# Kernel optimization log

Hardware: AMD Instinct MI355X
Metric: run time of the kernel (lower is better)

Reference implementation:

```python
import jax, jax.numpy as jnp
import numpy as np

B, T, C = 2, 2048, 1024
H = 16
HD = C // H  # head_size = 64


def setup_inputs() -> dict:
    key = jax.random.key(0)
    k1, k2, k3 = jax.random.split(key, 3)
    x = jax.random.normal(k1, (B, T, C), dtype=jnp.float32)
    W_qkv = jax.random.normal(k2, (C, 3 * C), dtype=jnp.float32) * (1.0 / np.sqrt(C))
    b_qkv = jnp.zeros((3 * C,), dtype=jnp.float32)
    W_proj = jax.random.normal(k3, (C, C), dtype=jnp.float32) * (1.0 / np.sqrt(C))
    b_proj = jnp.zeros((C,), dtype=jnp.float32)
    return {"x": x, "W_qkv": W_qkv, "b_qkv": b_qkv, "W_proj": W_proj, "b_proj": b_proj}


def reference(x, W_qkv, b_qkv, W_proj, b_proj):
    Bc, Tc, Cc = x.shape
    qkv = x @ W_qkv + b_qkv                      # [B,T,3C]
    # Faithful to torch: view(B,T,H,3*HD) then chunk(3,-1) -> per-head interleaved split
    qkv = qkv.reshape(Bc, Tc, H, 3 * HD)
    q = qkv[..., 0 * HD:1 * HD]                  # [B,T,H,HD]
    k = qkv[..., 1 * HD:2 * HD]
    v = qkv[..., 2 * HD:3 * HD]
    # scores: [B,H,T,T]
    att = jnp.einsum('bqhd,bkhd->bhqk', q, k) / np.sqrt(HD)
    causal = jnp.tril(jnp.ones((Tc, Tc), dtype=bool))
    att = jnp.where(causal[None, None, :, :], att, -jnp.inf)
    att = jax.nn.softmax(att, axis=-1)
    out = jnp.einsum('bhqk,bkhd->bqhd', att, v).reshape(Bc, Tc, Cc)
    return out @ W_proj + b_proj
```

## Files before the change

### kernel.cpp

```cpp
#include <hip/hip_runtime.h>
#include <hip/hip_bf16.h>
#include <stdint.h>
#include <math.h>

#define T_SEQ 2048
#define NHEAD 16
#define CDIM 1024
#define QKV2_LD 2048

typedef __attribute__((ext_vector_type(8))) short short8;
typedef __attribute__((ext_vector_type(4))) short short4v;
typedef __attribute__((ext_vector_type(4))) float floatx4;

static __device__ __forceinline__ short bf16b(float f) {
    __hip_bfloat16 h = __float2bfloat16(f);
    return __builtin_bit_cast(short, h);
}

__device__ __forceinline__ void transpose_body(
    const float* __restrict__ in, __hip_bfloat16* __restrict__ out,
    int R, int C, int bx, int by, int tid)
{
    __shared__ short tile[64][65];
    const int r0 = by << 6;
    const int c0 = bx << 6;
    #pragma unroll
    for (int t = 0; t < 4; ++t) {
        int ch = t * 256 + tid;
        int rr = ch >> 4, cc = (ch & 15) << 2;
        float4 v = *(const float4*)(in + (size_t)(r0 + rr) * C + c0 + cc);
        tile[rr][cc + 0] = bf16b(v.x);
        tile[rr][cc + 1] = bf16b(v.y);
        tile[rr][cc + 2] = bf16b(v.z);
        tile[rr][cc + 3] = bf16b(v.w);
    }
    __syncthreads();
    #pragma unroll
    for (int t = 0; t < 2; ++t) {
        int ch = t * 256 + tid;
        int cc = ch >> 3, rr8 = (ch & 7) << 3;
        short8 v;
        #pragma unroll
        for (int j = 0; j < 8; ++j) v[j] = tile[rr8 + j][cc];
        *(short8*)(out + (size_t)(c0 + cc) * R + r0 + rr8) = v;
    }
}

__global__ __launch_bounds__(256) void prep_kernel(
    const float* __restrict__ x,     __hip_bfloat16* __restrict__ xb,
    const float* __restrict__ Wqkv,  __hip_bfloat16* __restrict__ WqkvT,
    const float* __restrict__ Wproj, __hip_bfloat16* __restrict__ WprojT)
{
    const int bid = blockIdx.x;
    const int tid = threadIdx.x;
    if (bid < 2048) {
        int i = (bid * 256 + tid) * 8;
        float4 a = *(const float4*)(x + i);
        float4 b = *(const float4*)(x + i + 4);
        short8 o;
        o[0] = bf16b(a.x); o[1] = bf16b(a.y); o[2] = bf16b(a.z); o[3] = bf16b(a.w);
        o[4] = bf16b(b.x); o[5] = bf16b(b.y); o[6] = bf16b(b.z); o[7] = bf16b(b.w);
        *(short8*)(xb + i) = o;
    } else if (bid < 2816) {
        int r = bid - 2048;
        transpose_body(Wqkv, WqkvT, 1024, 3072, r % 48, r / 48, tid);
    } else {
        int r = bid - 2816;
        transpose_body(Wproj, WprojT, 1024, 1024, r & 15, r >> 4, tid);
    }
}

template <int MI, int NI, int MINW, bool QKV, typename OutT>
__global__ __launch_bounds__(256, MINW) void gemm_bias_kernel(
    const __hip_bfloat16* __restrict__ A,
    const __hip_bfloat16* __restrict__ Bt,
    const float* __restrict__ bias,
    OutT* __restrict__ C,
    __hip_bfloat16* __restrict__ vT,
    int M, int N, int K)
{
    __shared__ short As[MI * 32 * 64];
    __shared__ short Bs[NI * 32 * 64];
    const int tid  = threadIdx.x;
    const int lane = tid & 63;
    const int w    = tid >> 6;
    const int quad = lane >> 4;
    const int c16  = lane & 15;
    const int m0 = blockIdx.x * (MI * 32);
    const int n0 = blockIdx.y * (NI * 32);
    const int wm = (w >> 1) * (MI * 16);
    const int wn = (w & 1) * (NI * 16);

    floatx4 acc[MI][NI] = {};

    for (int kt = 0; kt < K; kt += 64) {
        __syncthreads();
        #pragma unroll
        for (int r = 0; r < MI; ++r) {
            int ch = r * 256 + tid;
            int row = ch >> 3, k8 = (ch & 7) << 3;
            const __hip_bfloat16* ga = A + (size_t)(m0 + row) * K + kt + k8;
            __builtin_amdgcn_global_load_lds(
                (const __attribute__((address_space(1))) void*)ga,
                (__attribute__((address_space(3))) void*)&As[ch * 8], 16, 0, 0);
        }
        #pragma unroll
        for (int r = 0; r < NI; ++r) {
            int ch = r * 256 + tid;
            int row = ch >> 3, k8 = (ch & 7) << 3;
            const __hip_bfloat16* gb = Bt + (size_t)(n0 + row) * K + kt + k8;
            __builtin_amdgcn_global_load_lds(
                (const __attribute__((address_space(1))) void*)gb,
                (__attribute__((address_space(3))) void*)&Bs[ch * 8], 16, 0, 0);
        }
        __syncthreads();
        #pragma unroll
        for (int ko = 0; ko < 64; ko += 32) {
            short8 af[MI], bfr[NI];
            #pragma unroll
            for (int mi = 0; mi < MI; ++mi)
                af[mi] = *(const short8*)&As[(wm + mi * 16 + c16) * 64 + ko + quad * 8];
            #pragma unroll
            for (int ni = 0; ni < NI; ++ni)
                bfr[ni] = *(const short8*)&Bs[(wn + ni * 16 + c16) * 64 + ko + quad * 8];
            #pragma unroll
            for (int mi = 0; mi < MI; ++mi)
                #pragma unroll
                for (int ni = 0; ni < NI; ++ni)
                    acc[mi][ni] = __builtin_amdgcn_mfma_f32_16x16x32_bf16(
                        af[mi], bfr[ni], acc[mi][ni], 0, 0, 0);
        }
    }

    if constexpr (QKV) {
        const int colblk = (n0 + wn) >> 6;
        const int head = colblk / 3;
        const int kind = colblk % 3;
        const int b    = m0 >> 11;
        __syncthreads();
        if (kind == 2) {
            short* tp = (w < 2) ? &As[w * 4096] : &Bs[(w - 2) * 4096];
            #pragma unroll
            for (int mi = 0; mi < MI; ++mi)
                #pragma unroll
                for (int ni = 0; ni < NI; ++ni) {
                    int hd = ni * 16 + c16;
                    float bv = bias[n0 + wn + hd];
                    short4v pk;
                    #pragma unroll
                    for (int r2 = 0; r2 < 4; ++r2) pk[r2] = bf16b(acc[mi][ni][r2] + bv);
                    int tc = mi * 4 + quad;
                    *(short4v*)&tp[hd * 64 + ((tc ^ ((hd & 7) << 1)) << 2)] = pk;
                }
            const size_t vb2 = ((size_t)(b * 16 + head)) * 64 * T_SEQ;
            const int t0 = (m0 + wm) & 2047;
            #pragma unroll
            for (int it = 0; it < 8; ++it) {
                int hd = it * 8 + (lane >> 3);
                int tc2 = (lane & 7) << 1;
                short8 vv = *(const short8*)&tp[hd * 64 + ((tc2 ^ ((hd & 7) << 1)) << 2)];
                *(short8*)(vT + vb2 + (size_t)hd * T_SEQ + t0 + ((lane & 7) << 3)) = vv;
            }
        } else {
            const int cbase = head * 128 + kind * 64;
            #pragma unroll
            for (int mi = 0; mi < MI; ++mi)
                #pragma unroll
                for (int ni = 0; ni < NI; ++ni) {
                    float bv = bias[n0 + wn + ni * 16 + c16];
                    int col = cbase + ni * 16 + c16;
                    #pragma unroll
                    for (int r2 = 0; r2 < 4; ++r2) {
                        int row = m0 + wm + mi * 16 + quad * 4 + r2;
                        C[(size_t)row * QKV2_LD + col] = __float2bfloat16(acc[mi][ni][r2] + bv);
                    }
                }
        }
    } else {
        #pragma unroll
        for (int mi = 0; mi < MI; ++mi)
            #pragma unroll
            for (int ni = 0; ni < NI; ++ni) {
                int col = n0 + wn + ni * 16 + c16;
                float bv = bias[col];
                #pragma unroll
                for (int r2 = 0; r2 < 4; ++r2) {
                    int row = m0 + wm + mi * 16 + quad * 4 + r2;
                    float v = acc[mi][ni][r2] + bv;
                    if constexpr (__is_same(OutT, float)) {
                        C[(size_t)row * N + col] = v;
                    } else {
                        C[(size_t)row * N + col] = __float2bfloat16(v);
                    }
                }
            }
    }
}

__global__ __launch_bounds__(256, 4) void attn_kernel(
    const __hip_bfloat16* __restrict__ qkv,
    const __hip_bfloat16* __restrict__ vT,
    __hip_bfloat16* __restrict__ attn_out)
{
    __shared__ short Ks[2][64 * 64];
    __shared__ short Vs[2][64 * 64];
    __shared__ short Pl[4][16 * 64];

    const int hb = blockIdx.x;
    const int qt = 31 - blockIdx.y;
    const int h  = hb & 15;
    const int b  = hb >> 4;
    const int tid  = threadIdx.x;
    const int lane = tid & 63;
    const int w    = tid >> 6;
    const int quad = lane >> 4;
    const int c16  = lane & 15;

    const size_t rowbase = (size_t)b * T_SEQ;
    const size_t vbase   = (size_t)hb * 64 * T_SEQ;
    const int q0   = qt << 6;
    const int wrow = w << 4;
    const int hoff = h * 128;
    const int key  = c16 & 7;

    short8 qf[2];
    #pragma unroll
    for (int ko = 0; ko < 2; ++ko)
        qf[ko] = *(const short8*)(qkv +
            (rowbase + q0 + wrow + c16) * QKV2_LD + hoff + ko * 32 + quad * 8);

    floatx4 O[4] = {};
    float lp = 0.f;
    const float sc = 0.125f * 1.4426950408889634f;
    const int nkt = qt + 1;

    auto stage = [&](int kt, int bsel) {
        const int k0s = kt << 6;
        #pragma unroll
        for (int r = 0; r < 2; ++r) {
            int ch = r * 256 + tid;
            int krow = ch >> 3;
            int hc = (ch & 7) ^ (krow & 7);
            const __hip_bfloat16* g = qkv + (rowbase + k0s + krow) * QKV2_LD + hoff + 64 + hc * 8;
            __builtin_amdgcn_global_load_lds(
                (const __attribute__((address_space(1))) void*)g,
                (__attribute__((address_space(3))) void*)&Ks[bsel][ch * 8], 16, 0, 0);
        }
        #pragma unroll
        for (int r = 0; r < 2; ++r) {
            int ch = r * 256 + tid;
            int hd = ch >> 3;
            int kc = (ch & 7) ^ (hd & 7);
            const __hip_bfloat16* g = vT + vbase + (size_t)hd * T_SEQ + k0s + kc * 8;
            __builtin_amdgcn_global_load_lds(
                (const __attribute__((address_space(1))) void*)g,
                (__attribute__((address_space(3))) void*)&Vs[bsel][ch * 8], 16, 0, 0);
        }
    };

    stage(0, 0);
    int buf = 0;

    for (int kt = 0; kt < nkt; ++kt) {
        __syncthreads();
        if (kt + 1 < nkt) stage(kt + 1, buf ^ 1);

        short8 kf[2][4], vb[2][4];
        #pragma unroll
        for (int ko = 0; ko < 2; ++ko)
            #pragma unroll
            for (int ni = 0; ni < 4; ++ni) {
                int sl = ((4 * ko + quad) ^ key) << 3;
                kf[ko][ni] = *(const short8*)&Ks[buf][(ni * 16 + c16) * 64 + sl];
                vb[ko][ni] = *(const short8*)&Vs[buf][(ni * 16 + c16) * 64 + sl];
            }

        short* Pw = &Pl[w][0];
        floatx4 S[4] = {};
        #pragma unroll
        for (int ko = 0; ko < 2; ++ko)
            #pragma unroll
            for (int ni = 0; ni < 4; ++ni)
                S[ni] = __builtin_amdgcn_mfma_f32_16x16x32_bf16(
                    kf[ko][ni], qf[ko], S[ni], 0, 0, 0);

        if (kt == qt) {
            #pragma unroll
            for (int ni = 0; ni < 4; ++ni)
                #pragma unroll
                for (int r = 0; r < 4; ++r) {
                    bool msk = (ni * 16 + quad * 4 + r) > (wrow + c16);
                    float pe = msk ? 0.f : exp2f(S[ni][r] * sc);
                    S[ni][r] = pe;
                    lp += pe;
                }
        } else {
            #pragma unroll
            for (int ni = 0; ni < 4; ++ni)
                #pragma unroll
                for (int r = 0; r < 4; ++r) {
                    float pe = exp2f(S[ni][r] * sc);
                    S[ni][r] = pe;
                    lp += pe;
                }
        }

        #pragma unroll
        for (int ni = 0; ni < 4; ++ni) {
            short4v pk;
            #pragma unroll
            for (int r = 0; r < 4; ++r) pk[r] = bf16b(S[ni][r]);
            int pair = ni * 2 + (quad >> 1);
            int off = c16 * 64 + ((((pair ^ key) << 1) + (quad & 1)) << 2);
            *(short4v*)&Pw[off] = pk;
        }

        #pragma unroll
        for (int ko = 0; ko < 2; ++ko) {
            int off = c16 * 64 + (((ko * 4 + quad) ^ key) << 3);
            short8 pa = *(const short8*)&Pw[off];
            #pragma unroll
            for (int ni = 0; ni < 4; ++ni)
                O[ni] = __builtin_amdgcn_mfma_f32_16x16x32_bf16(
                    vb[ko][ni], pa, O[ni], 0, 0, 0);
        }
        buf ^= 1;
    }

    float l = lp;
    l += __shfl_xor(l, 16);
    l += __shfl_xor(l, 32);
    float inv = 1.0f / l;
    size_t row = rowbase + q0 + wrow + c16;
    #pragma unroll
    for (int ni = 0; ni < 4; ++ni) {
        short4v o;
        #pragma unroll
        for (int r = 0; r < 4; ++r) o[r] = bf16b(O[ni][r] * inv);
        *(short4v*)(attn_out + row * CDIM + h * 64 + ni * 16 + quad * 4) = o;
    }
}

extern "C" void kernel_launch(void* const* d_in, const int* in_sizes, int n_in,
                              void* d_out, int out_size, void* d_ws, size_t ws_size,
                              hipStream_t stream) {
    const float* x     = (const float*)d_in[0];
    const float* Wqkv  = (const float*)d_in[1];
    const float* bqkv  = (const float*)d_in[2];
    const float* Wproj = (const float*)d_in[3];
    const float* bproj = (const float*)d_in[4];
    float* out = (float*)d_out;

    __hip_bfloat16* xb     = (__hip_bfloat16*)d_ws;
    __hip_bfloat16* WqkvT  = xb     + (size_t)4096 * 1024;
    __hip_bfloat16* WprojT = WqkvT  + (size_t)3072 * 1024;
    __hip_bfloat16* qkv2   = WprojT + (size_t)1024 * 1024;
    __hip_bfloat16* vT     = qkv2   + (size_t)4096 * 2048;
    __hip_bfloat16* attn   = vT     + (size_t)32 * 64 * 2048;

    prep_kernel<<<3072, 256, 0, stream>>>(x, xb, Wqkv, WqkvT, Wproj, WprojT);
    gemm_bias_kernel<4, 4, 2, true, __hip_bfloat16>
        <<<dim3(4096 / 128, 3072 / 128), 256, 0, stream>>>(
        xb, WqkvT, bqkv, qkv2, vT, 4096, 3072, 1024);
    attn_kernel<<<dim3(32, 32), 256, 0, stream>>>(qkv2, vT, attn);
    gemm_bias_kernel<2, 2, 4, false, float>
        <<<dim3(4096 / 64, 1024 / 64), 256, 0, stream>>>(
        attn, WprojT, bproj, out, nullptr, 4096, 1024, 1024);
}
```

Baseline: 178.4 us.

## Fold softmax scale into Q, pass P through permlane swaps, retune attention schedule

Multiplies Q by the softmax scale times log2(e) in the QKV GEMM epilogue, which removes the per-score multiply before exp2. The P tile now goes from the score layout to the MFMA operand layout with packed bf16 converts and permlane32/16 swaps instead of a round trip through LDS, which frees the P shared buffer. The change also raises launch bounds to 5 waves, reorders query tiles into interleaved ascending and descending groups for load balance, adds s_setprio around the MFMA blocks, splits the row-sum accumulator into four, and retiles the output projection GEMM. Rounding Q after the scale changes numerics slightly, and the higher occupancy target may force register spills.

```diff
diff --git a/kernel.cpp b/kernel.cpp
--- a/kernel.cpp
+++ b/kernel.cpp
@@ -11,6 +11,8 @@
 typedef __attribute__((ext_vector_type(8))) short short8;
 typedef __attribute__((ext_vector_type(4))) short short4v;
 typedef __attribute__((ext_vector_type(4))) float floatx4;
+typedef __attribute__((ext_vector_type(2))) unsigned int uint2v;
+typedef __attribute__((ext_vector_type(4))) unsigned int uint4v;
 
 static __device__ __forceinline__ short bf16b(float f) {
     __hip_bfloat16 h = __float2bfloat16(f);
@@ -163,6 +165,7 @@
             }
         } else {
             const int cbase = head * 128 + kind * 64;
+            const float qsc = (kind == 0) ? 0.18033688011112042f : 1.0f;
             #pragma unroll
             for (int mi = 0; mi < MI; ++mi)
                 #pragma unroll
@@ -172,7 +175,8 @@
                     #pragma unroll
                     for (int r2 = 0; r2 < 4; ++r2) {
                         int row = m0 + wm + mi * 16 + quad * 4 + r2;
-                        C[(size_t)row * QKV2_LD + col] = __float2bfloat16(acc[mi][ni][r2] + bv);
+                        C[(size_t)row * QKV2_LD + col] =
+                            __float2bfloat16((acc[mi][ni][r2] + bv) * qsc);
                     }
                 }
         }
@@ -197,17 +201,17 @@
     }
 }
 
-__global__ __launch_bounds__(256, 4) void attn_kernel(
+__global__ __launch_bounds__(256, 5) void attn_kernel(
     const __hip_bfloat16* __restrict__ qkv,
     const __hip_bfloat16* __restrict__ vT,
     __hip_bfloat16* __restrict__ attn_out)
 {
     __shared__ short Ks[2][64 * 64];
     __shared__ short Vs[2][64 * 64];
-    __shared__ short Pl[4][16 * 64];
 
     const int hb = blockIdx.x;
-    const int qt = 31 - blockIdx.y;
+    const int yj = blockIdx.y & 7, yk = blockIdx.y >> 3;
+    const int qt = (yk & 1) ? ((yk & 2 ? 31 : 15) - yj) : ((yk & 2 ? 16 : 0) + yj);
     const int h  = hb & 15;
     const int b  = hb >> 4;
     const int tid  = threadIdx.x;
@@ -230,8 +234,7 @@
             (rowbase + q0 + wrow + c16) * QKV2_LD + hoff + ko * 32 + quad * 8);
 
     floatx4 O[4] = {};
-    float lp = 0.f;
-    const float sc = 0.125f * 1.4426950408889634f;
+    floatx4 lp4 = {};
     const int nkt = qt + 1;
 
     auto stage = [&](int kt, int bsel) {
@@ -275,14 +278,15 @@
                 vb[ko][ni] = *(const short8*)&Vs[buf][(ni * 16 + c16) * 64 + sl];
             }
 
-        short* Pw = &Pl[w][0];
         floatx4 S[4] = {};
+        __builtin_amdgcn_s_setprio(1);
         #pragma unroll
         for (int ko = 0; ko < 2; ++ko)
             #pragma unroll
             for (int ni = 0; ni < 4; ++ni)
                 S[ni] = __builtin_amdgcn_mfma_f32_16x16x32_bf16(
                     kf[ko][ni], qf[ko], S[ni], 0, 0, 0);
+        __builtin_amdgcn_s_setprio(0);
 
         if (kt == qt) {
             #pragma unroll
@@ -290,44 +294,51 @@
                 #pragma unroll
                 for (int r = 0; r < 4; ++r) {
                     bool msk = (ni * 16 + quad * 4 + r) > (wrow + c16);
-                    float pe = msk ? 0.f : exp2f(S[ni][r] * sc);
+                    float pe = msk ? 0.f : exp2f(S[ni][r]);
                     S[ni][r] = pe;
-                    lp += pe;
+                    lp4[r] += pe;
                 }
         } else {
             #pragma unroll
             for (int ni = 0; ni < 4; ++ni)
                 #pragma unroll
                 for (int r = 0; r < 4; ++r) {
-                    float pe = exp2f(S[ni][r] * sc);
+                    float pe = exp2f(S[ni][r]);
                     S[ni][r] = pe;
-                    lp += pe;
-                }
-        }
-
+                    lp4[r] += pe;
+                }
+        }
+
+        unsigned pw[4][2];
         #pragma unroll
         for (int ni = 0; ni < 4; ++ni) {
-            short4v pk;
-            #pragma unroll
-            for (int r = 0; r < 4; ++r) pk[r] = bf16b(S[ni][r]);
-            int pair = ni * 2 + (quad >> 1);
-            int off = c16 * 64 + ((((pair ^ key) << 1) + (quad & 1)) << 2);
-            *(short4v*)&Pw[off] = pk;
+            asm("v_cvt_pk_bf16_f32 %0, %1, %2"
+                : "=v"(pw[ni][0]) : "v"(S[ni][0]), "v"(S[ni][1]));
+            asm("v_cvt_pk_bf16_f32 %0, %1, %2"
+                : "=v"(pw[ni][1]) : "v"(S[ni][2]), "v"(S[ni][3]));
         }
 
         #pragma unroll
         for (int ko = 0; ko < 2; ++ko) {
-            int off = c16 * 64 + (((ko * 4 + quad) ^ key) << 3);
-            short8 pa = *(const short8*)&Pw[off];
+            uint4v pb;
+            uint2v t0 = __builtin_amdgcn_permlane32_swap(pw[2 * ko][0], pw[2 * ko + 1][0], false, false);
+            uint2v u0 = __builtin_amdgcn_permlane16_swap(t0[0], t0[1], false, false);
+            uint2v t1 = __builtin_amdgcn_permlane32_swap(pw[2 * ko][1], pw[2 * ko + 1][1], false, false);
+            uint2v u1 = __builtin_amdgcn_permlane16_swap(t1[0], t1[1], false, false);
+            pb[0] = u0[0]; pb[2] = u0[1];
+            pb[1] = u1[0]; pb[3] = u1[1];
+            short8 pa = __builtin_bit_cast(short8, pb);
+            __builtin_amdgcn_s_setprio(1);
             #pragma unroll
             for (int ni = 0; ni < 4; ++ni)
                 O[ni] = __builtin_amdgcn_mfma_f32_16x16x32_bf16(
                     vb[ko][ni], pa, O[ni], 0, 0, 0);
+            __builtin_amdgcn_s_setprio(0);
         }
         buf ^= 1;
     }
 
-    float l = lp;
+    float l = lp4[0] + lp4[1] + lp4[2] + lp4[3];
     l += __shfl_xor(l, 16);
     l += __shfl_xor(l, 32);
     float inv = 1.0f / l;
@@ -363,7 +374,7 @@
         <<<dim3(4096 / 128, 3072 / 128), 256, 0, stream>>>(
         xb, WqkvT, bqkv, qkv2, vT, 4096, 3072, 1024);
     attn_kernel<<<dim3(32, 32), 256, 0, stream>>>(qkv2, vT, attn);
-    gemm_bias_kernel<2, 2, 4, false, float>
-        <<<dim3(4096 / 64, 1024 / 64), 256, 0, stream>>>(
+    gemm_bias_kernel<4, 2, 2, false, float>
+        <<<dim3(4096 / 128, 1024 / 64), 256, 0, stream>>>(
         attn, WprojT, bproj, out, nullptr, 4096, 1024, 1024);
 }
```

Result: slower. 232.9 us (+30.5%).
